# Kernel tuning notes

Measured on AMD Instinct MI355X. Metric: run time of the kernel, lower is better.

The kernel has to match this reference:

```python
import jax, jax.numpy as jnp
import numpy as np

NH, KD, VD, C = 8, 64, 64, 256

def conv1x1(x, w, b):
    # x: (B,C,D,H,W), w: (O,C), b: (O,)
    return jnp.einsum('bcdhw,oc->bodhw', x, w) + b[None, :, None, None, None]

def setup_inputs() -> dict:
    key = jax.random.key(0)
    ks = jax.random.split(key, 8)
    B, D, H, W = 2, 32, 32, 32
    s = 0.02
    return {
        'x': jax.random.normal(ks[0], (B, C, D, H, W), jnp.float32),
        'q_w': jax.random.normal(ks[1], (NH * KD, C), jnp.float32) * s,
        'q_b': jnp.zeros((NH * KD,), jnp.float32),
        'kv_w': jax.random.normal(ks[2], (KD + VD, C), jnp.float32) * s,
        'kv_b': jnp.zeros((KD + VD,), jnp.float32),
        'proj_w': jax.random.normal(ks[3], (C, NH * VD), jnp.float32) * s,
        'proj_b': jnp.zeros((C,), jnp.float32),
        'layer_scale': jnp.full((C, 1, 1, 1), 1e-5, jnp.float32),
    }

def reference(x, q_w, q_b, kv_w, kv_b, proj_w, proj_b, layer_scale):
    B, Cc, D, H, W = x.shape
    scale = VD ** -0.5
    # q: (B, nh, D, H, W, kd) -> flatten(3,5) -> (B, nh, D, H*W*kd)
    q = conv1x1(x, q_w, q_b).reshape(B, NH, KD, D, H, W).transpose(0, 1, 3, 4, 5, 2)
    q = q.reshape(B, NH, D, H * W * KD)
    kv = conv1x1(x, kv_w, kv_b)  # (B, kd+vd, D, H, W)
    k = kv[:, :KD].transpose(0, 2, 3, 4, 1).reshape(B, D, H * W * KD)  # shared across heads
    v = kv[:, KD:].transpose(0, 2, 3, 4, 1).reshape(B, D, H * W * VD)
    attn = jax.nn.softmax(jnp.einsum('bnqf,bkf->bnqk', q, k) * scale, axis=-1)  # (B,nh,D,D)
    o = jnp.einsum('bnqk,bkf->bnqf', attn, v)  # (B, nh, D, H*W*vd)
    # transpose(1,2) then row-major reshape, exactly as torch
    o = o.transpose(0, 2, 1, 3).reshape(B, D, H, W, NH * VD).transpose(0, 4, 1, 2, 3)
    out = conv1x1(o, proj_w, proj_b)
    return out * layer_scale[None]
```

## Files before the change

### kernel.cpp

```cpp
#include <hip/hip_runtime.h>
#include <math.h>

#define SS 32768

typedef _Float16 half4v __attribute__((ext_vector_type(4)));
typedef _Float16 half8v __attribute__((ext_vector_type(8)));
typedef float float4v __attribute__((ext_vector_type(4)));

__device__ __forceinline__ void gload16(const void* g, void* l) {
    __builtin_amdgcn_global_load_lds(
        (const __attribute__((address_space(1))) unsigned int*)g,
        (__attribute__((address_space(3))) unsigned int*)l, 16, 0, 0);
}

__global__ __launch_bounds__(256)
void cvt_x_kernel(const float* __restrict__ x, _Float16* __restrict__ x_t)
{
    __shared__ float ls[64][65];
    const int b = blockIdx.z, c0 = blockIdx.y * 64, s0 = blockIdx.x * 64;
    const int t = threadIdx.x;
    const int tr = t >> 4, tc = t & 15;
#pragma unroll
    for (int p = 0; p < 4; p++) {
        int c_l = p * 16 + tr;
        float4v v = *(const float4v*)(x + (size_t)(b * 256 + c0 + c_l) * SS + s0 + tc * 4);
        ls[c_l][tc * 4 + 0] = v.x;
        ls[c_l][tc * 4 + 1] = v.y;
        ls[c_l][tc * 4 + 2] = v.z;
        ls[c_l][tc * 4 + 3] = v.w;
    }
    __syncthreads();
#pragma unroll
    for (int p = 0; p < 4; p++) {
        int s_l = p * 16 + tr;
        half4v h;
        h.x = (_Float16)ls[tc * 4 + 0][s_l];
        h.y = (_Float16)ls[tc * 4 + 1][s_l];
        h.z = (_Float16)ls[tc * 4 + 2][s_l];
        h.w = (_Float16)ls[tc * 4 + 3][s_l];
        *(half4v*)(x_t + ((size_t)b * SS + s0 + s_l) * 256 + c0 + tc * 4) = h;
    }
}

__global__ __launch_bounds__(256)
void cvt_w_kernel(const float* __restrict__ src, _Float16* __restrict__ dst)
{
    int i = (blockIdx.x * 256 + threadIdx.x) * 4;
    float4v v = *(const float4v*)(src + i);
    half4v h;
    h.x = (_Float16)v.x; h.y = (_Float16)v.y; h.z = (_Float16)v.z; h.w = (_Float16)v.w;
    *(half4v*)(dst + i) = h;
}

__global__ __launch_bounds__(256)
void conv_mfma_kernel(const _Float16* __restrict__ x_t,
                      const _Float16* __restrict__ wq,
                      const _Float16* __restrict__ wkv,
                      const float* __restrict__ q_b,
                      const float* __restrict__ kv_b,
                      _Float16* __restrict__ q_t,
                      _Float16* __restrict__ kv_t)
{
    __shared__ _Float16 Ws[128 * 32];
    __shared__ _Float16 Xs[128 * 32];
    const int b = blockIdx.y;
    const int s_tile = blockIdx.x / 5;
    const int o_tile = blockIdx.x % 5;
    const int s0 = s_tile * 128;
    const bool is_q = (o_tile < 4);
    const _Float16* W = is_q ? wq : wkv;
    const float* bias = is_q ? q_b : kv_b;
    const int od0 = is_q ? o_tile * 128 : 0;
    const int ODST = is_q ? 512 : 128;
    _Float16* dst = is_q ? q_t : kv_t;

    const int t = threadIdx.x;
    const int w = t >> 6, l = t & 63;
    const int om = (w & 1) * 64, sn = (w >> 1) * 64;

    float4v acc[4][4];
#pragma unroll
    for (int i = 0; i < 4; i++)
#pragma unroll
        for (int j = 0; j < 4; j++) acc[i][j] = (float4v){0.f, 0.f, 0.f, 0.f};

    const _Float16* wg0 = W + (size_t)(od0 + 32 * w + (l >> 2)) * 256 + (l & 3) * 8;
    const _Float16* xg0 = x_t + ((size_t)b * SS + s0 + 32 * w + (l >> 2)) * 256 + (l & 3) * 8;
    _Float16* wl = &Ws[(32 * w) * 32];
    _Float16* xl = &Xs[(32 * w) * 32];

    for (int c0 = 0; c0 < 256; c0 += 32) {
        gload16(wg0 + c0, wl);
        gload16(wg0 + 16 * 256 + c0, wl + 16 * 32);
        gload16(xg0 + c0, xl);
        gload16(xg0 + 16 * 256 + c0, xl + 16 * 32);
        __syncthreads();
        half8v a[4], bb[4];
#pragma unroll
        for (int i = 0; i < 4; i++)
            a[i] = *(const half8v*)&Ws[(om + i * 16 + (l & 15)) * 32 + (l >> 4) * 8];
#pragma unroll
        for (int j = 0; j < 4; j++)
            bb[j] = *(const half8v*)&Xs[(sn + j * 16 + (l & 15)) * 32 + (l >> 4) * 8];
#pragma unroll
        for (int i = 0; i < 4; i++)
#pragma unroll
            for (int j = 0; j < 4; j++)
                acc[i][j] = __builtin_amdgcn_mfma_f32_16x16x32_f16(a[i], bb[j], acc[i][j], 0, 0, 0);
        __syncthreads();
    }
    const int qd = l >> 4, m = l & 15;
#pragma unroll
    for (int i = 0; i < 4; i++) {
        float bv[4];
#pragma unroll
        for (int r = 0; r < 4; r++) bv[r] = bias[od0 + om + i * 16 + qd * 4 + r];
#pragma unroll
        for (int j = 0; j < 4; j++) {
            half4v h;
            h.x = (_Float16)(acc[i][j].x + bv[0]);
            h.y = (_Float16)(acc[i][j].y + bv[1]);
            h.z = (_Float16)(acc[i][j].z + bv[2]);
            h.w = (_Float16)(acc[i][j].w + bv[3]);
            size_t s = (size_t)b * SS + s0 + sn + j * 16 + m;
            *(half4v*)(dst + s * ODST + od0 + om + i * 16 + qd * 4) = h;
        }
    }
}

__global__ __launch_bounds__(256)
void logits_mfma_kernel(const _Float16* __restrict__ q_t,
                        const _Float16* __restrict__ kv_t,
                        float* __restrict__ Lbuf)
{
    __shared__ _Float16 Qs[32 * 64];
    __shared__ _Float16 Ks[32 * 64];
    const int hwc = blockIdx.x, nh = blockIdx.y, b = blockIdx.z;
    const int t = threadIdx.x, w = t >> 6, l = t & 63;
    const int mi = (w & 1) * 16, nj = (w >> 1) * 16;

    const int rhalf = w & 1;
    const bool isK = (w >> 1) != 0;
    const int rrow = rhalf * 16 + (l >> 3);
    const int ch = l & 7;
    _Float16* lbase = (isK ? Ks : Qs) + (rhalf * 16) * 64;

    float4v acc = (float4v){0.f, 0.f, 0.f, 0.f};

    for (int hh = 0; hh < 32; hh++) {
        const int hw = hwc * 32 + hh;
        if (!isK) {
            const _Float16* g = q_t + ((size_t)b * SS + (size_t)rrow * 1024 + hw) * 512 + nh * 64 + ch * 8;
            gload16(g, lbase);
            gload16(g + (size_t)8 * 1024 * 512, lbase + 8 * 64);
        } else {
            const _Float16* g = kv_t + ((size_t)b * SS + (size_t)rrow * 1024 + hw) * 128 + ch * 8;
            gload16(g, lbase);
            gload16(g + (size_t)8 * 1024 * 128, lbase + 8 * 64);
        }
        __syncthreads();
#pragma unroll
        for (int ks = 0; ks < 2; ks++) {
            half8v a = *(const half8v*)&Qs[(mi + (l & 15)) * 64 + ks * 32 + (l >> 4) * 8];
            half8v bb = *(const half8v*)&Ks[(nj + (l & 15)) * 64 + ks * 32 + (l >> 4) * 8];
            acc = __builtin_amdgcn_mfma_f32_16x16x32_f16(a, bb, acc, 0, 0, 0);
        }
        __syncthreads();
    }
    float* Lb = Lbuf + (size_t)(b * 8 + nh) * 1024;
    const int row = mi + (l >> 4) * 4, col = nj + (l & 15);
#pragma unroll
    for (int rr = 0; rr < 4; rr++)
        atomicAdd(&Lb[(row + rr) * 32 + col], acc[rr]);
}

__global__ __launch_bounds__(256)
void softmax_kernel(float* __restrict__ Lbuf)
{
    int r = blockIdx.x * 256 + threadIdx.x;
    if (r >= 512) return;
    float* row = Lbuf + (size_t)r * 32;
    float p[32];
#pragma unroll
    for (int j = 0; j < 32; j++) p[j] = row[j];
    float m = p[0];
#pragma unroll
    for (int j = 1; j < 32; j++) m = fmaxf(m, p[j]);
    float s = 0.f;
#pragma unroll
    for (int j = 0; j < 32; j++) { p[j] = expf((p[j] - m) * 0.125f); s += p[j]; }
    float inv = 1.f / s;
#pragma unroll
    for (int j = 0; j < 32; j++) row[j] = p[j] * inv;
}

__global__ __launch_bounds__(256)
void attn_v_kernel(const _Float16* __restrict__ kv_t,
                   const float* __restrict__ attn,
                   _Float16* __restrict__ o_t)
{
    __shared__ float as_[8 * 32 * 32];
    const int wq = blockIdx.x, hl = blockIdx.y, b = blockIdx.z;
    const int t = threadIdx.x;
    {
        const float* src = attn + (size_t)b * 8192;
#pragma unroll
        for (int ll = 0; ll < 8; ll++) {
            int idx = (t + ll * 256) * 4;
            *(float4v*)(&as_[idx]) = *(const float4v*)(src + idx);
        }
    }
    __syncthreads();
    const int q4 = t & 127;
    const int half = t >> 7;
    const int tt = q4 >> 4;
    const int vd = (q4 * 4) & 63;
    const int hw = hl * 256 + wq * 8 + tt;
    float4v vreg[32];
#pragma unroll
    for (int j = 0; j < 32; j++) {
        half4v hv = *(const half4v*)(kv_t + ((size_t)((b * 32 + j) * 1024 + hw)) * 128 + 64 + vd);
        vreg[j] = (float4v){(float)hv.x, (float)hv.y, (float)hv.z, (float)hv.w};
    }
    _Float16* outb = o_t + (size_t)b * SS * 512;
#pragma unroll 2
    for (int rr = 0; rr < 128; rr++) {
        int row = half * 128 + rr;
        int hh = row >> 5, d = row & 31;
        const float* arow = &as_[row * 32];
        float ax = 0.f, ay = 0.f, az = 0.f, aw = 0.f;
#pragma unroll
        for (int j4 = 0; j4 < 8; j4++) {
            float4v a4 = *(const float4v*)(&arow[j4 * 4]);
            float4v v0 = vreg[j4 * 4 + 0];
            float4v v1 = vreg[j4 * 4 + 1];
            float4v v2 = vreg[j4 * 4 + 2];
            float4v v3 = vreg[j4 * 4 + 3];
            ax = fmaf(a4.x, v0.x, ax); ay = fmaf(a4.x, v0.y, ay);
            az = fmaf(a4.x, v0.z, az); aw = fmaf(a4.x, v0.w, aw);
            ax = fmaf(a4.y, v1.x, ax); ay = fmaf(a4.y, v1.y, ay);
            az = fmaf(a4.y, v1.z, az); aw = fmaf(a4.y, v1.w, aw);
            ax = fmaf(a4.z, v2.x, ax); ay = fmaf(a4.z, v2.y, ay);
            az = fmaf(a4.z, v2.z, az); aw = fmaf(a4.z, v2.w, aw);
            ax = fmaf(a4.w, v3.x, ax); ay = fmaf(a4.w, v3.y, ay);
            az = fmaf(a4.w, v3.z, az); aw = fmaf(a4.w, v3.w, aw);
        }
        int hp = hh * 4 + hl;
        size_t sp = (size_t)d * 1024 + hp * 32 + wq;
        half4v o4;
        o4.x = (_Float16)ax; o4.y = (_Float16)ay; o4.z = (_Float16)az; o4.w = (_Float16)aw;
        *(half4v*)(outb + sp * 512 + q4 * 4) = o4;
    }
}

__global__ __launch_bounds__(256)
void proj_mfma_kernel(const _Float16* __restrict__ o_t,
                      const _Float16* __restrict__ wp,
                      const float* __restrict__ pb,
                      const float* __restrict__ ls,
                      float* __restrict__ out)
{
    __shared__ _Float16 Ws[128 * 32];
    __shared__ _Float16 Xs[128 * 32];
    const int b = blockIdx.y;
    const int s_tile = blockIdx.x >> 1;
    const int o_tile = blockIdx.x & 1;
    const int s0 = s_tile * 128, o0 = o_tile * 128;
    const int t = threadIdx.x;
    const int w = t >> 6, l = t & 63;
    const int om = (w & 1) * 64, sn = (w >> 1) * 64;

    float4v acc[4][4];
#pragma unroll
    for (int i = 0; i < 4; i++)
#pragma unroll
        for (int j = 0; j < 4; j++) acc[i][j] = (float4v){0.f, 0.f, 0.f, 0.f};

    const _Float16* wg0 = wp + (size_t)(o0 + 32 * w + (l >> 2)) * 512 + (l & 3) * 8;
    const _Float16* xg0 = o_t + ((size_t)b * SS + s0 + 32 * w + (l >> 2)) * 512 + (l & 3) * 8;
    _Float16* wl = &Ws[(32 * w) * 32];
    _Float16* xl = &Xs[(32 * w) * 32];

    for (int c0 = 0; c0 < 512; c0 += 32) {
        gload16(wg0 + c0, wl);
        gload16(wg0 + 16 * 512 + c0, wl + 16 * 32);
        gload16(xg0 + c0, xl);
        gload16(xg0 + 16 * 512 + c0, xl + 16 * 32);
        __syncthreads();
        half8v a[4], bb[4];
#pragma unroll
        for (int i = 0; i < 4; i++)
            a[i] = *(const half8v*)&Ws[(om + i * 16 + (l & 15)) * 32 + (l >> 4) * 8];
#pragma unroll
        for (int j = 0; j < 4; j++)
            bb[j] = *(const half8v*)&Xs[(sn + j * 16 + (l & 15)) * 32 + (l >> 4) * 8];
#pragma unroll
        for (int i = 0; i < 4; i++)
#pragma unroll
            for (int j = 0; j < 4; j++)
                acc[i][j] = __builtin_amdgcn_mfma_f32_16x16x32_f16(a[i], bb[j], acc[i][j], 0, 0, 0);
        __syncthreads();
    }
    const int qd = l >> 4, m = l & 15;
#pragma unroll
    for (int i = 0; i < 4; i++) {
        float pbv[4], lsv[4];
#pragma unroll
        for (int r = 0; r < 4; r++) {
            int o = o0 + om + i * 16 + qd * 4 + r;
            pbv[r] = pb[o];
            lsv[r] = ls[o];
        }
#pragma unroll
        for (int j = 0; j < 4; j++) {
            int s = s0 + sn + j * 16 + m;
#pragma unroll
            for (int r = 0; r < 4; r++) {
                int o = o0 + om + i * 16 + qd * 4 + r;
                out[((size_t)b * 256 + o) * SS + s] = (acc[i][j][r] + pbv[r]) * lsv[r];
            }
        }
    }
}

extern "C" void kernel_launch(void* const* d_in, const int* in_sizes, int n_in,
                              void* d_out, int out_size, void* d_ws, size_t ws_size,
                              hipStream_t stream)
{
    const float* x      = (const float*)d_in[0];
    const float* q_w    = (const float*)d_in[1];
    const float* q_b    = (const float*)d_in[2];
    const float* kv_w   = (const float*)d_in[3];
    const float* kv_b   = (const float*)d_in[4];
    const float* proj_w = (const float*)d_in[5];
    const float* proj_b = (const float*)d_in[6];
    const float* ls     = (const float*)d_in[7];
    float* out = (float*)d_out;

    char* ws = (char*)d_ws;
    _Float16* x_t  = (_Float16*)(ws);
    _Float16* q_t  = (_Float16*)(ws + 33554432);
    _Float16* kv_t = (_Float16*)(ws + 100663296);
    float*    Lbuf = (float*)   (ws + 117440512);
    _Float16* wq   = (_Float16*)(ws + 117506048);
    _Float16* wkv  = (_Float16*)(ws + 117768192);
    _Float16* wp   = (_Float16*)(ws + 117833728);
    _Float16* o_t  = q_t;

    hipMemsetAsync(Lbuf, 0, 65536, stream);

    cvt_x_kernel<<<dim3(512, 4, 2), 256, 0, stream>>>(x, x_t);
    cvt_w_kernel<<<dim3(128), 256, 0, stream>>>(q_w, wq);
    cvt_w_kernel<<<dim3(32),  256, 0, stream>>>(kv_w, wkv);
    cvt_w_kernel<<<dim3(128), 256, 0, stream>>>(proj_w, wp);

    conv_mfma_kernel<<<dim3(256 * 5, 2), 256, 0, stream>>>(x_t, wq, wkv, q_b, kv_b, q_t, kv_t);
    logits_mfma_kernel<<<dim3(32, 8, 2), 256, 0, stream>>>(q_t, kv_t, Lbuf);
    softmax_kernel<<<dim3(2), 256, 0, stream>>>(Lbuf);
    attn_v_kernel<<<dim3(32, 4, 2), 256, 0, stream>>>(kv_t, Lbuf, o_t);
    proj_mfma_kernel<<<dim3(256 * 2, 2), 256, 0, stream>>>(o_t, wp, proj_b, ls, out);
}
```

Before: 284.2 us.

## Deepen GEMM K-tiles with swizzled LDS, rework logits reduction, fuse weight casts

The conv and proj GEMMs now stage 64-wide K chunks per barrier, with an XOR-like rotated LDS layout to avoid bank conflicts, and remap block indices so s-tiles sharing weights run close together. The logits kernel drops the LDS staging and atomics: it loads Q/K fragments directly into registers, reduces across waves in shared memory and writes per-chunk partials. Softmax then sums those partials, which removes the memset. The three weight-cast launches are merged into one. The changes cut barrier count and launch overhead, in exchange for a larger LDS footprint and a heavier softmax pass.

```diff
diff --git a/kernel.cpp b/kernel.cpp
--- a/kernel.cpp
+++ b/kernel.cpp
@@ -43,13 +43,20 @@
 }
 
 __global__ __launch_bounds__(256)
-void cvt_w_kernel(const float* __restrict__ src, _Float16* __restrict__ dst)
-{
-    int i = (blockIdx.x * 256 + threadIdx.x) * 4;
-    float4v v = *(const float4v*)(src + i);
+void cvt_w3_kernel(const float* __restrict__ s0, _Float16* __restrict__ d0,
+                   const float* __restrict__ s1, _Float16* __restrict__ d1,
+                   const float* __restrict__ s2, _Float16* __restrict__ d2)
+{
+    int bx = blockIdx.x;
+    const float* s; _Float16* d; int base;
+    if (bx < 128)      { s = s0; d = d0; base = bx; }
+    else if (bx < 160) { s = s1; d = d1; base = bx - 128; }
+    else               { s = s2; d = d2; base = bx - 160; }
+    int i = (base * 256 + threadIdx.x) * 4;
+    float4v v = *(const float4v*)(s + i);
     half4v h;
     h.x = (_Float16)v.x; h.y = (_Float16)v.y; h.z = (_Float16)v.z; h.w = (_Float16)v.w;
-    *(half4v*)(dst + i) = h;
+    *(half4v*)(d + i) = h;
 }
 
 __global__ __launch_bounds__(256)
@@ -61,11 +68,13 @@
                       _Float16* __restrict__ q_t,
                       _Float16* __restrict__ kv_t)
 {
-    __shared__ _Float16 Ws[128 * 32];
-    __shared__ _Float16 Xs[128 * 32];
+    __shared__ _Float16 Ws[128 * 64];
+    __shared__ _Float16 Xs[128 * 64];
     const int b = blockIdx.y;
-    const int s_tile = blockIdx.x / 5;
-    const int o_tile = blockIdx.x % 5;
+    const int bx = blockIdx.x;
+    const int grp = bx / 40, rem = bx % 40;
+    const int s_tile = grp * 8 + (rem & 7);
+    const int o_tile = rem >> 3;
     const int s0 = s_tile * 128;
     const bool is_q = (o_tile < 4);
     const _Float16* W = is_q ? wq : wkv;
@@ -78,35 +87,46 @@
     const int w = t >> 6, l = t & 63;
     const int om = (w & 1) * 64, sn = (w >> 1) * 64;
 
+    const int lr = l >> 3;
+    const int gch = ((l & 7) - lr) & 7;
+    const int m15 = l & 15;
+    const int sl0 = ((((l >> 4) + (l & 7)) & 7)) * 8;
+    const int sl1 = ((((l >> 4) + 4 + (l & 7)) & 7)) * 8;
+
     float4v acc[4][4];
 #pragma unroll
     for (int i = 0; i < 4; i++)
 #pragma unroll
         for (int j = 0; j < 4; j++) acc[i][j] = (float4v){0.f, 0.f, 0.f, 0.f};
 
-    const _Float16* wg0 = W + (size_t)(od0 + 32 * w + (l >> 2)) * 256 + (l & 3) * 8;
-    const _Float16* xg0 = x_t + ((size_t)b * SS + s0 + 32 * w + (l >> 2)) * 256 + (l & 3) * 8;
-    _Float16* wl = &Ws[(32 * w) * 32];
-    _Float16* xl = &Xs[(32 * w) * 32];
-
-    for (int c0 = 0; c0 < 256; c0 += 32) {
-        gload16(wg0 + c0, wl);
-        gload16(wg0 + 16 * 256 + c0, wl + 16 * 32);
-        gload16(xg0 + c0, xl);
-        gload16(xg0 + 16 * 256 + c0, xl + 16 * 32);
+    const _Float16* wg = W + (size_t)(od0 + 32 * w + lr) * 256 + gch * 8;
+    const _Float16* xg = x_t + ((size_t)b * SS + s0 + 32 * w + lr) * 256 + gch * 8;
+    _Float16* wl = &Ws[(32 * w) * 64];
+    _Float16* xl = &Xs[(32 * w) * 64];
+
+    for (int c0 = 0; c0 < 256; c0 += 64) {
+#pragma unroll
+        for (int rb = 0; rb < 4; rb++) {
+            gload16(wg + (size_t)rb * 8 * 256 + c0, wl + rb * 8 * 64);
+            gload16(xg + (size_t)rb * 8 * 256 + c0, xl + rb * 8 * 64);
+        }
         __syncthreads();
-        half8v a[4], bb[4];
-#pragma unroll
-        for (int i = 0; i < 4; i++)
-            a[i] = *(const half8v*)&Ws[(om + i * 16 + (l & 15)) * 32 + (l >> 4) * 8];
-#pragma unroll
-        for (int j = 0; j < 4; j++)
-            bb[j] = *(const half8v*)&Xs[(sn + j * 16 + (l & 15)) * 32 + (l >> 4) * 8];
-#pragma unroll
-        for (int i = 0; i < 4; i++)
+#pragma unroll
+        for (int ks = 0; ks < 2; ks++) {
+            const int sl = ks ? sl1 : sl0;
+            half8v a[4], bb[4];
+#pragma unroll
+            for (int i = 0; i < 4; i++)
+                a[i] = *(const half8v*)&Ws[(om + i * 16 + m15) * 64 + sl];
 #pragma unroll
             for (int j = 0; j < 4; j++)
-                acc[i][j] = __builtin_amdgcn_mfma_f32_16x16x32_f16(a[i], bb[j], acc[i][j], 0, 0, 0);
+                bb[j] = *(const half8v*)&Xs[(sn + j * 16 + m15) * 64 + sl];
+#pragma unroll
+            for (int i = 0; i < 4; i++)
+#pragma unroll
+                for (int j = 0; j < 4; j++)
+                    acc[i][j] = __builtin_amdgcn_mfma_f32_16x16x32_f16(a[i], bb[j], acc[i][j], 0, 0, 0);
+        }
         __syncthreads();
     }
     const int qd = l >> 4, m = l & 15;
@@ -129,69 +149,96 @@
 }
 
 __global__ __launch_bounds__(256)
-void logits_mfma_kernel(const _Float16* __restrict__ q_t,
-                        const _Float16* __restrict__ kv_t,
-                        float* __restrict__ Lbuf)
-{
-    __shared__ _Float16 Qs[32 * 64];
-    __shared__ _Float16 Ks[32 * 64];
+void logits_kernel(const _Float16* __restrict__ q_t,
+                   const _Float16* __restrict__ kv_t,
+                   float* __restrict__ Lpart)
+{
+    __shared__ float red[4][1024];
     const int hwc = blockIdx.x, nh = blockIdx.y, b = blockIdx.z;
     const int t = threadIdx.x, w = t >> 6, l = t & 63;
-    const int mi = (w & 1) * 16, nj = (w >> 1) * 16;
-
-    const int rhalf = w & 1;
-    const bool isK = (w >> 1) != 0;
-    const int rrow = rhalf * 16 + (l >> 3);
-    const int ch = l & 7;
-    _Float16* lbase = (isK ? Ks : Qs) + (rhalf * 16) * 64;
-
-    float4v acc = (float4v){0.f, 0.f, 0.f, 0.f};
-
-    for (int hh = 0; hh < 32; hh++) {
-        const int hw = hwc * 32 + hh;
-        if (!isK) {
-            const _Float16* g = q_t + ((size_t)b * SS + (size_t)rrow * 1024 + hw) * 512 + nh * 64 + ch * 8;
-            gload16(g, lbase);
-            gload16(g + (size_t)8 * 1024 * 512, lbase + 8 * 64);
-        } else {
-            const _Float16* g = kv_t + ((size_t)b * SS + (size_t)rrow * 1024 + hw) * 128 + ch * 8;
-            gload16(g, lbase);
-            gload16(g + (size_t)8 * 1024 * 128, lbase + 8 * 64);
-        }
-        __syncthreads();
-#pragma unroll
-        for (int ks = 0; ks < 2; ks++) {
-            half8v a = *(const half8v*)&Qs[(mi + (l & 15)) * 64 + ks * 32 + (l >> 4) * 8];
-            half8v bb = *(const half8v*)&Ks[(nj + (l & 15)) * 64 + ks * 32 + (l >> 4) * 8];
-            acc = __builtin_amdgcn_mfma_f32_16x16x32_f16(a, bb, acc, 0, 0, 0);
-        }
-        __syncthreads();
-    }
-    float* Lb = Lbuf + (size_t)(b * 8 + nh) * 1024;
-    const int row = mi + (l >> 4) * 4, col = nj + (l & 15);
-#pragma unroll
-    for (int rr = 0; rr < 4; rr++)
-        atomicAdd(&Lb[(row + rr) * 32 + col], acc[rr]);
-}
-
-__global__ __launch_bounds__(256)
-void softmax_kernel(float* __restrict__ Lbuf)
+    const int m = l & 15, c8 = (l >> 4) * 8;
+    float4v acc[2][2];
+#pragma unroll
+    for (int i = 0; i < 2; i++)
+#pragma unroll
+        for (int j = 0; j < 2; j++) acc[i][j] = (float4v){0.f, 0.f, 0.f, 0.f};
+
+    const _Float16* qb0 = q_t + (size_t)b * SS * 512 + nh * 64 + c8;
+    const _Float16* kb0 = kv_t + (size_t)b * SS * 128 + c8;
+#pragma unroll 4
+    for (int hh = 0; hh < 8; hh++) {
+        const int hw = hwc * 32 + w * 8 + hh;
+        const _Float16* qr0 = qb0 + ((size_t)m * 1024 + hw) * 512;
+        const _Float16* qr1 = qb0 + ((size_t)(m + 16) * 1024 + hw) * 512;
+        const _Float16* kr0 = kb0 + ((size_t)m * 1024 + hw) * 128;
+        const _Float16* kr1 = kb0 + ((size_t)(m + 16) * 1024 + hw) * 128;
+        half8v a0l = *(const half8v*)(qr0);
+        half8v a0h = *(const half8v*)(qr0 + 32);
+        half8v a1l = *(const half8v*)(qr1);
+        half8v a1h = *(const half8v*)(qr1 + 32);
+        half8v b0l = *(const half8v*)(kr0);
+        half8v b0h = *(const half8v*)(kr0 + 32);
+        half8v b1l = *(const half8v*)(kr1);
+        half8v b1h = *(const half8v*)(kr1 + 32);
+        acc[0][0] = __builtin_amdgcn_mfma_f32_16x16x32_f16(a0l, b0l, acc[0][0], 0, 0, 0);
+        acc[0][0] = __builtin_amdgcn_mfma_f32_16x16x32_f16(a0h, b0h, acc[0][0], 0, 0, 0);
+        acc[0][1] = __builtin_amdgcn_mfma_f32_16x16x32_f16(a0l, b1l, acc[0][1], 0, 0, 0);
+        acc[0][1] = __builtin_amdgcn_mfma_f32_16x16x32_f16(a0h, b1h, acc[0][1], 0, 0, 0);
+        acc[1][0] = __builtin_amdgcn_mfma_f32_16x16x32_f16(a1l, b0l, acc[1][0], 0, 0, 0);
+        acc[1][0] = __builtin_amdgcn_mfma_f32_16x16x32_f16(a1h, b0h, acc[1][0], 0, 0, 0);
+        acc[1][1] = __builtin_amdgcn_mfma_f32_16x16x32_f16(a1l, b1l, acc[1][1], 0, 0, 0);
+        acc[1][1] = __builtin_amdgcn_mfma_f32_16x16x32_f16(a1h, b1h, acc[1][1], 0, 0, 0);
+    }
+    const int rbase = (l >> 4) * 4;
+#pragma unroll
+    for (int qi = 0; qi < 2; qi++)
+#pragma unroll
+        for (int qj = 0; qj < 2; qj++)
+#pragma unroll
+            for (int rr = 0; rr < 4; rr++)
+                red[w][(qi * 16 + rbase + rr) * 32 + qj * 16 + m] = acc[qi][qj][rr];
+    __syncthreads();
+    float4v v = *(const float4v*)&red[0][t * 4];
+    v += *(const float4v*)&red[1][t * 4];
+    v += *(const float4v*)&red[2][t * 4];
+    v += *(const float4v*)&red[3][t * 4];
+    *(float4v*)(Lpart + (((size_t)hwc * 2 + b) * 8 + nh) * 1024 + t * 4) = v;
+}
+
+__global__ __launch_bounds__(256)
+void softmax_kernel(const float* __restrict__ Lpart, float* __restrict__ Lsm)
 {
     int r = blockIdx.x * 256 + threadIdx.x;
-    if (r >= 512) return;
-    float* row = Lbuf + (size_t)r * 32;
-    float p[32];
-#pragma unroll
-    for (int j = 0; j < 32; j++) p[j] = row[j];
-    float m = p[0];
-#pragma unroll
-    for (int j = 1; j < 32; j++) m = fmaxf(m, p[j]);
+    float4v p[8];
+#pragma unroll
+    for (int j4 = 0; j4 < 8; j4++) p[j4] = (float4v){0.f, 0.f, 0.f, 0.f};
+    for (int hwc = 0; hwc < 32; hwc++) {
+        const float* src = Lpart + (size_t)hwc * 16384 + (size_t)r * 32;
+#pragma unroll
+        for (int j4 = 0; j4 < 8; j4++) p[j4] += *(const float4v*)(src + j4 * 4);
+    }
+    float mx = p[0].x;
+#pragma unroll
+    for (int j4 = 0; j4 < 8; j4++) {
+        mx = fmaxf(mx, p[j4].x); mx = fmaxf(mx, p[j4].y);
+        mx = fmaxf(mx, p[j4].z); mx = fmaxf(mx, p[j4].w);
+    }
     float s = 0.f;
 #pragma unroll
-    for (int j = 0; j < 32; j++) { p[j] = expf((p[j] - m) * 0.125f); s += p[j]; }
+    for (int j4 = 0; j4 < 8; j4++) {
+        p[j4].x = expf((p[j4].x - mx) * 0.125f); s += p[j4].x;
+        p[j4].y = expf((p[j4].y - mx) * 0.125f); s += p[j4].y;
+        p[j4].z = expf((p[j4].z - mx) * 0.125f); s += p[j4].z;
+        p[j4].w = expf((p[j4].w - mx) * 0.125f); s += p[j4].w;
+    }
     float inv = 1.f / s;
-#pragma unroll
-    for (int j = 0; j < 32; j++) row[j] = p[j] * inv;
+    float* dst = Lsm + (size_t)r * 32;
+#pragma unroll
+    for (int j4 = 0; j4 < 8; j4++) {
+        float4v o = p[j4];
+        o.x *= inv; o.y *= inv; o.z *= inv; o.w *= inv;
+        *(float4v*)(dst + j4 * 4) = o;
+    }
 }
 
 __global__ __launch_bounds__(256)
@@ -260,45 +307,58 @@
                       const float* __restrict__ ls,
                       float* __restrict__ out)
 {
-    __shared__ _Float16 Ws[128 * 32];
-    __shared__ _Float16 Xs[128 * 32];
+    __shared__ _Float16 Ws[128 * 64];
+    __shared__ _Float16 Xs[128 * 64];
     const int b = blockIdx.y;
-    const int s_tile = blockIdx.x >> 1;
-    const int o_tile = blockIdx.x & 1;
+    const int bx = blockIdx.x;
+    const int grp = bx >> 4, rem = bx & 15;
+    const int s_tile = grp * 8 + (rem & 7);
+    const int o_tile = rem >> 3;
     const int s0 = s_tile * 128, o0 = o_tile * 128;
     const int t = threadIdx.x;
     const int w = t >> 6, l = t & 63;
     const int om = (w & 1) * 64, sn = (w >> 1) * 64;
 
+    const int lr = l >> 3;
+    const int gch = ((l & 7) - lr) & 7;
+    const int m15 = l & 15;
+    const int sl0 = ((((l >> 4) + (l & 7)) & 7)) * 8;
+    const int sl1 = ((((l >> 4) + 4 + (l & 7)) & 7)) * 8;
+
     float4v acc[4][4];
 #pragma unroll
     for (int i = 0; i < 4; i++)
 #pragma unroll
         for (int j = 0; j < 4; j++) acc[i][j] = (float4v){0.f, 0.f, 0.f, 0.f};
 
-    const _Float16* wg0 = wp + (size_t)(o0 + 32 * w + (l >> 2)) * 512 + (l & 3) * 8;
-    const _Float16* xg0 = o_t + ((size_t)b * SS + s0 + 32 * w + (l >> 2)) * 512 + (l & 3) * 8;
-    _Float16* wl = &Ws[(32 * w) * 32];
-    _Float16* xl = &Xs[(32 * w) * 32];
-
-    for (int c0 = 0; c0 < 512; c0 += 32) {
-        gload16(wg0 + c0, wl);
-        gload16(wg0 + 16 * 512 + c0, wl + 16 * 32);
-        gload16(xg0 + c0, xl);
-        gload16(xg0 + 16 * 512 + c0, xl + 16 * 32);
+    const _Float16* wg = wp + (size_t)(o0 + 32 * w + lr) * 512 + gch * 8;
+    const _Float16* xg = o_t + ((size_t)b * SS + s0 + 32 * w + lr) * 512 + gch * 8;
+    _Float16* wl = &Ws[(32 * w) * 64];
+    _Float16* xl = &Xs[(32 * w) * 64];
+
+    for (int c0 = 0; c0 < 512; c0 += 64) {
+#pragma unroll
+        for (int rb = 0; rb < 4; rb++) {
+            gload16(wg + (size_t)rb * 8 * 512 + c0, wl + rb * 8 * 64);
+            gload16(xg + (size_t)rb * 8 * 512 + c0, xl + rb * 8 * 64);
+        }
         __syncthreads();
-        half8v a[4], bb[4];
-#pragma unroll
-        for (int i = 0; i < 4; i++)
-            a[i] = *(const half8v*)&Ws[(om + i * 16 + (l & 15)) * 32 + (l >> 4) * 8];
-#pragma unroll
-        for (int j = 0; j < 4; j++)
-            bb[j] = *(const half8v*)&Xs[(sn + j * 16 + (l & 15)) * 32 + (l >> 4) * 8];
-#pragma unroll
-        for (int i = 0; i < 4; i++)
+#pragma unroll
+        for (int ks = 0; ks < 2; ks++) {
+            const int sl = ks ? sl1 : sl0;
+            half8v a[4], bb[4];
+#pragma unroll
+            for (int i = 0; i < 4; i++)
+                a[i] = *(const half8v*)&Ws[(om + i * 16 + m15) * 64 + sl];
 #pragma unroll
             for (int j = 0; j < 4; j++)
-                acc[i][j] = __builtin_amdgcn_mfma_f32_16x16x32_f16(a[i], bb[j], acc[i][j], 0, 0, 0);
+                bb[j] = *(const half8v*)&Xs[(sn + j * 16 + m15) * 64 + sl];
+#pragma unroll
+            for (int i = 0; i < 4; i++)
+#pragma unroll
+                for (int j = 0; j < 4; j++)
+                    acc[i][j] = __builtin_amdgcn_mfma_f32_16x16x32_f16(a[i], bb[j], acc[i][j], 0, 0, 0);
+        }
         __syncthreads();
     }
     const int qd = l >> 4, m = l & 15;
@@ -341,22 +401,19 @@
     _Float16* x_t  = (_Float16*)(ws);
     _Float16* q_t  = (_Float16*)(ws + 33554432);
     _Float16* kv_t = (_Float16*)(ws + 100663296);
-    float*    Lbuf = (float*)   (ws + 117440512);
-    _Float16* wq   = (_Float16*)(ws + 117506048);
-    _Float16* wkv  = (_Float16*)(ws + 117768192);
-    _Float16* wp   = (_Float16*)(ws + 117833728);
+    float*    Lpart= (float*)   (ws + 117440512);
+    float*    Lsm  = (float*)   (ws + 119537664);
+    _Float16* wq   = (_Float16*)(ws + 119603200);
+    _Float16* wkv  = (_Float16*)(ws + 119865344);
+    _Float16* wp   = (_Float16*)(ws + 119930880);
     _Float16* o_t  = q_t;
 
-    hipMemsetAsync(Lbuf, 0, 65536, stream);
-
     cvt_x_kernel<<<dim3(512, 4, 2), 256, 0, stream>>>(x, x_t);
-    cvt_w_kernel<<<dim3(128), 256, 0, stream>>>(q_w, wq);
-    cvt_w_kernel<<<dim3(32),  256, 0, stream>>>(kv_w, wkv);
-    cvt_w_kernel<<<dim3(128), 256, 0, stream>>>(proj_w, wp);
-
-    conv_mfma_kernel<<<dim3(256 * 5, 2), 256, 0, stream>>>(x_t, wq, wkv, q_b, kv_b, q_t, kv_t);
-    logits_mfma_kernel<<<dim3(32, 8, 2), 256, 0, stream>>>(q_t, kv_t, Lbuf);
-    softmax_kernel<<<dim3(2), 256, 0, stream>>>(Lbuf);
-    attn_v_kernel<<<dim3(32, 4, 2), 256, 0, stream>>>(kv_t, Lbuf, o_t);
-    proj_mfma_kernel<<<dim3(256 * 2, 2), 256, 0, stream>>>(o_t, wp, proj_b, ls, out);
-}
+    cvt_w3_kernel<<<dim3(288), 256, 0, stream>>>(q_w, wq, kv_w, wkv, proj_w, wp);
+
+    conv_mfma_kernel<<<dim3(1280, 2), 256, 0, stream>>>(x_t, wq, wkv, q_b, kv_b, q_t, kv_t);
+    logits_kernel<<<dim3(32, 8, 2), 256, 0, stream>>>(q_t, kv_t, Lpart);
+    softmax_kernel<<<dim3(2), 256, 0, stream>>>(Lpart, Lsm);
+    attn_v_kernel<<<dim3(32, 4, 2), 256, 0, stream>>>(kv_t, Lsm, o_t);
+    proj_mfma_kernel<<<dim3(512, 2), 256, 0, stream>>>(o_t, wp, proj_b, ls, out);
+}
```

Measured after the change: 291.1 us. +2.4%, slower.
